# Kernel optimization log

Hardware: AMD Instinct MI355X
Metric: run time of the kernel (lower is better)

Reference implementation:

```python
import jax, jax.numpy as jnp
import numpy as np

B, T, D1, D2, DM, V, K = 2, 512, 256, 128, 1024, 32000, 4
SCALE = 0.05  # keep tanh/sigmoid out of full saturation with randn params


def setup_inputs() -> dict:
    key = jax.random.key(0)
    ks = jax.random.split(key, 7)
    s = lambda k, shape: SCALE * jax.random.normal(k, shape, dtype=jnp.float32)
    return {
        "gc": jax.random.normal(ks[0], (B, T, D1), dtype=jnp.float32),
        "H": s(ks[1], (K, DM, D1)),
        "U": s(ks[2], (K, D2, D1)),
        "v": s(ks[3], (V, D2)),
        "u": s(ks[4], (K, D1)),
        "b": s(ks[5], (V, K)),
        "emb": s(ks[6], (V, DM)),
    }


def reference(gc, H, U, v, u, b, emb):
    # gc: (B,T,D1)
    hc = jnp.tanh(jnp.einsum('kdi,bti->btkd', H, gc))        # (B,T,K,DM)
    tU = jnp.tanh(jnp.einsum('kji,bti->btkj', U, gc))        # (B,T,K,D2)
    # token- and context-dependent gate logits: (B,T,V,K)
    lc = (jnp.einsum('vj,btkj->btvk', v, tU)
          + jnp.einsum('ki,bti->btk', u, gc)[:, :, None, :]
          + b[None, None])
    gamma = jax.nn.sigmoid(lc[..., :K - 1])                  # (B,T,V,3)
    g0, g1, g2 = gamma[..., 0], gamma[..., 1], gamma[..., 2]
    # sigmoid-tree mixture priors: (B,T,V,K)
    pi = jnp.stack([g0 * g1, g0 * (1.0 - g1),
                    (1.0 - g0) * g2, (1.0 - g0) * (1.0 - g2)], axis=-1)
    # contract hc with embeddings per gate FIRST (avoids btikj blow-up),
    # then weight by pi -- same math as the original pi (x) emb outer product.
    dots = jnp.einsum('btkd,vd->btvk', hc, emb)              # (B,T,V,K)
    logits = jnp.sum(pi * dots, axis=-1)                     # (B,T,V)
    return jax.nn.softmax(logits, axis=-1)
```

## Files before the change

### kernel.cpp

```cpp
#include <hip/hip_runtime.h>
#include <math.h>

namespace {

typedef _Float16 f16;
typedef _Float16 f16x8 __attribute__((ext_vector_type(8)));
typedef float    f32x4 __attribute__((ext_vector_type(4)));

constexpr int kBT = 1024, kD1 = 256, kD2 = 128, kDM = 1024, kV = 32000, kK = 4;
constexpr int AR = kBT * kK;
constexpr int ROWS_H = kK * kDM;
constexpr int ROWS_U = kK * kD2;
constexpr int ROWS_ALL = ROWS_H + ROWS_U + kK;
constexpr int HALF_ROWS = ROWS_ALL / 2;

__global__ __launch_bounds__(256) void prep_gemm(
    const float* __restrict__ gc, const float* __restrict__ Hm,
    const float* __restrict__ Um, const float* __restrict__ um,
    f16* __restrict__ hc, f16* __restrict__ tu, float* __restrict__ ug)
{
    __shared__ float sgc[8][kD1];
    const int btBase = blockIdx.x * 8;
    for (int idx = threadIdx.x; idx < 8 * kD1; idx += 256)
        sgc[idx / kD1][idx % kD1] = gc[(size_t)btBase * kD1 + idx];
    __syncthreads();

    const int rStart = blockIdx.y * HALF_ROWS;
    const int rEnd   = rStart + HALF_ROWS;
    for (int r = rStart + (int)threadIdx.x; r < rEnd; r += 256) {
        const float* wrow;
        if (r < ROWS_H)               wrow = Hm + (size_t)r * kD1;
        else if (r < ROWS_H + ROWS_U) wrow = Um + (size_t)(r - ROWS_H) * kD1;
        else                          wrow = um + (size_t)(r - ROWS_H - ROWS_U) * kD1;

        float acc[8] = {0.f,0.f,0.f,0.f,0.f,0.f,0.f,0.f};
        for (int i = 0; i < kD1; i += 4) {
            const float4 w = *reinterpret_cast<const float4*>(wrow + i);
            #pragma unroll
            for (int b = 0; b < 8; ++b) {
                const float4 g = *reinterpret_cast<const float4*>(&sgc[b][i]);
                acc[b] = fmaf(w.x, g.x, acc[b]);
                acc[b] = fmaf(w.y, g.y, acc[b]);
                acc[b] = fmaf(w.z, g.z, acc[b]);
                acc[b] = fmaf(w.w, g.w, acc[b]);
            }
        }
        #pragma unroll
        for (int b = 0; b < 8; ++b) {
            const int bt = btBase + b;
            if (r < ROWS_H) {
                const int k = r >> 10, d = r & 1023;
                hc[((size_t)(bt * kK + k) << 10) + d] = (f16)tanhf(acc[b]);
            } else if (r < ROWS_H + ROWS_U) {
                const int r2 = r - ROWS_H;
                const int k = r2 >> 7, j = r2 & 127;
                tu[(size_t)(bt * kK + k) * kD2 + j] = (f16)tanhf(acc[b]);
            } else {
                ug[bt * kK + (r - ROWS_H - ROWS_U)] = acc[b];
            }
        }
    }
}

__global__ __launch_bounds__(256) void cvt_kernel(
    const float* __restrict__ src, f16* __restrict__ dst, int n8)
{
    const int i = blockIdx.x * 256 + threadIdx.x;
    if (i >= n8) return;
    const float4 x0 = *reinterpret_cast<const float4*>(src + (size_t)i * 8);
    const float4 x1 = *reinterpret_cast<const float4*>(src + (size_t)i * 8 + 4);
    union { f16 h[8]; uint4 v; } u;
    u.h[0] = (f16)x0.x; u.h[1] = (f16)x0.y; u.h[2] = (f16)x0.z; u.h[3] = (f16)x0.w;
    u.h[4] = (f16)x1.x; u.h[5] = (f16)x1.y; u.h[6] = (f16)x1.z; u.h[7] = (f16)x1.w;
    *reinterpret_cast<uint4*>(dst + (size_t)i * 8) = u.v;
}

__global__ __launch_bounds__(256, 2) void fused_mfma(
    const f16* __restrict__ hc,  const f16* __restrict__ tu,
    const f16* __restrict__ v16, const f16* __restrict__ e16,
    const float* __restrict__ ug, const float* __restrict__ bmat,
    float* __restrict__ out)
{
    __shared__ __align__(16) f16 sA[128 * 64];
    __shared__ __align__(16) f16 sB[128 * 64];

    const int tid  = threadIdx.x;
    const int lane = tid & 63;
    const int wave = tid >> 6;
    const int fr = lane & 15, fq = lane >> 4;
    const int wrow = wave >> 1, wcol = wave & 1;
    const int aRowBase = blockIdx.x * 128;
    const int vBase    = blockIdx.y * 128;

    const int srow = lane >> 3;
    const int scol = ((lane & 7) ^ srow) * 8;

    auto stage = [&](const f16* __restrict__ g, f16* ldsbuf, int rowBase,
                     int stride, int dBase) {
        #pragma unroll
        for (int i = 0; i < 4; ++i) {
            const int c = wave * 4 + i;
            const f16* src = g + (size_t)(rowBase + c * 8 + srow) * stride + dBase + scol;
            f16* dst = ldsbuf + c * 512;
            __builtin_amdgcn_global_load_lds(
                (const __attribute__((address_space(1))) void*)src,
                (__attribute__((address_space(3))) void*)dst, 16, 0, 0);
        }
    };

    auto mmStep = [&](f32x4 (&acc)[4][4]) {
        #pragma unroll
        for (int kk = 0; kk < 2; ++kk) {
            f16x8 a[4], b[4];
            #pragma unroll
            for (int m = 0; m < 4; ++m) {
                const int r = wrow * 64 + m * 16 + fr;
                const int ps = (kk * 4 + fq) ^ (r & 7);
                a[m] = *reinterpret_cast<const f16x8*>(sA + r * 64 + ps * 8);
            }
            #pragma unroll
            for (int n = 0; n < 4; ++n) {
                const int r = wcol * 64 + n * 16 + fr;
                const int ps = (kk * 4 + fq) ^ (r & 7);
                b[n] = *reinterpret_cast<const f16x8*>(sB + r * 64 + ps * 8);
            }
            #pragma unroll
            for (int m = 0; m < 4; ++m)
                #pragma unroll
                for (int n = 0; n < 4; ++n)
                    acc[m][n] = __builtin_amdgcn_mfma_f32_16x16x32_f16(
                        a[m], b[n], acc[m][n], 0, 0, 0);
        }
    };

    f32x4 acc[4][4];
    const f32x4 zz = {0.f, 0.f, 0.f, 0.f};

    #pragma unroll
    for (int m = 0; m < 4; ++m)
        #pragma unroll
        for (int n = 0; n < 4; ++n) acc[m][n] = zz;

    for (int t = 0; t < kD2 / 64; ++t) {
        stage(tu,  sA, aRowBase, kD2, t * 64);
        stage(v16, sB, vBase,    kD2, t * 64);
        __syncthreads();
        mmStep(acc);
        __syncthreads();
    }

    float pi[4][4][4];
    #pragma unroll
    for (int m = 0; m < 4; ++m) {
        const int bt = blockIdx.x * 32 + wrow * 16 + m * 4 + fq;
        const float4 ugv = *reinterpret_cast<const float4*>(ug + bt * 4);
        #pragma unroll
        for (int n = 0; n < 4; ++n) {
            const int v = vBase + wcol * 64 + n * 16 + fr;
            const float4 bb = *reinterpret_cast<const float4*>(bmat + (size_t)v * 4);
            const float l0 = acc[m][n][0] + ugv.x + bb.x;
            const float l1 = acc[m][n][1] + ugv.y + bb.y;
            const float l2 = acc[m][n][2] + ugv.z + bb.z;
            const float g0 = 1.f / (1.f + __expf(-l0));
            const float g1 = 1.f / (1.f + __expf(-l1));
            const float g2 = 1.f / (1.f + __expf(-l2));
            pi[m][n][0] = g0 * g1;
            pi[m][n][1] = g0 * (1.f - g1);
            pi[m][n][2] = (1.f - g0) * g2;
            pi[m][n][3] = (1.f - g0) * (1.f - g2);
        }
    }

    #pragma unroll
    for (int m = 0; m < 4; ++m)
        #pragma unroll
        for (int n = 0; n < 4; ++n) acc[m][n] = zz;

    for (int t = 0; t < kDM / 64; ++t) {
        stage(hc,  sA, aRowBase, kDM, t * 64);
        stage(e16, sB, vBase,    kDM, t * 64);
        __syncthreads();
        mmStep(acc);
        __syncthreads();
    }

    #pragma unroll
    for (int m = 0; m < 4; ++m) {
        const int bt = blockIdx.x * 32 + wrow * 16 + m * 4 + fq;
        #pragma unroll
        for (int n = 0; n < 4; ++n) {
            const int v = vBase + wcol * 64 + n * 16 + fr;
            float lg = pi[m][n][0] * acc[m][n][0] + pi[m][n][1] * acc[m][n][1]
                     + pi[m][n][2] * acc[m][n][2] + pi[m][n][3] * acc[m][n][3];
            out[(size_t)bt * kV + v] = lg;
        }
    }
}

__global__ __launch_bounds__(256) void softmax_kernel(float* __restrict__ out)
{
    __shared__ float red[4];
    float* row = out + (size_t)blockIdx.x * kV;
    const int tid = threadIdx.x;

    float mx = -1e30f;
    for (int i = tid * 4; i < kV; i += 1024) {
        const float4 x = *reinterpret_cast<const float4*>(row + i);
        mx = fmaxf(mx, fmaxf(fmaxf(x.x, x.y), fmaxf(x.z, x.w)));
    }
    #pragma unroll
    for (int o = 1; o < 64; o <<= 1) mx = fmaxf(mx, __shfl_xor(mx, o));
    if ((tid & 63) == 0) red[tid >> 6] = mx;
    __syncthreads();
    mx = fmaxf(fmaxf(red[0], red[1]), fmaxf(red[2], red[3]));
    __syncthreads();

    float s = 0.f;
    for (int i = tid * 4; i < kV; i += 1024) {
        const float4 x = *reinterpret_cast<const float4*>(row + i);
        s += __expf(x.x - mx) + __expf(x.y - mx) + __expf(x.z - mx) + __expf(x.w - mx);
    }
    #pragma unroll
    for (int o = 1; o < 64; o <<= 1) s += __shfl_xor(s, o);
    if ((tid & 63) == 0) red[tid >> 6] = s;
    __syncthreads();
    s = red[0] + red[1] + red[2] + red[3];
    const float inv = 1.f / s;

    for (int i = tid * 4; i < kV; i += 1024) {
        const float4 x = *reinterpret_cast<const float4*>(row + i);
        float4 y;
        y.x = __expf(x.x - mx) * inv;
        y.y = __expf(x.y - mx) * inv;
        y.z = __expf(x.z - mx) * inv;
        y.w = __expf(x.w - mx) * inv;
        *reinterpret_cast<float4*>(row + i) = y;
    }
}

}

extern "C" void kernel_launch(void* const* d_in, const int* in_sizes, int n_in,
                              void* d_out, int out_size, void* d_ws, size_t ws_size,
                              hipStream_t stream)
{
    (void)in_sizes; (void)n_in; (void)out_size; (void)ws_size;
    const float* gc   = (const float*)d_in[0];
    const float* Hm   = (const float*)d_in[1];
    const float* Um   = (const float*)d_in[2];
    const float* vmat = (const float*)d_in[3];
    const float* um   = (const float*)d_in[4];
    const float* bmat = (const float*)d_in[5];
    const float* emb  = (const float*)d_in[6];
    float* out = (float*)d_out;

    size_t off = 0;
    auto take = [&](size_t bytes) -> char* {
        char* p = (char*)d_ws + off;
        off += (bytes + 255) & ~(size_t)255;
        return p;
    };
    f16*   hc  = (f16*)  take((size_t)AR * kDM * 2);
    f16*   tu  = (f16*)  take((size_t)AR * kD2 * 2);
    f16*   v16 = (f16*)  take((size_t)kV * kD2 * 2);
    f16*   e16 = (f16*)  take((size_t)kV * kDM * 2);
    float* ug  = (float*)take((size_t)AR * 4);

    prep_gemm<<<dim3(kBT / 8, 2), 256, 0, stream>>>(gc, Hm, Um, um, hc, tu, ug);
    cvt_kernel<<<(kV * kD2 / 8 + 255) / 256, 256, 0, stream>>>(vmat, v16, kV * kD2 / 8);
    cvt_kernel<<<(kV * kDM / 8 + 255) / 256, 256, 0, stream>>>(emb, e16, kV * kDM / 8);
    fused_mfma<<<dim3(AR / 128, kV / 128), 256, 0, stream>>>(
        hc, tu, v16, e16, ug, bmat, out);
    softmax_kernel<<<dim3(kBT), 256, 0, stream>>>(out);
}
```

Before: 576.4 us.

## Enlarge MFMA tiles to 256x256 with 4-stage async LDS pipeline and XCD remap

The fused GEMM kernel moves from 128x128 tiles with 256 threads to 256x256 tiles with 512 threads. The K-tile shrinks to 32 and a 4-buffer ring of global_load_lds transfers is prefetched two tiles ahead, with explicit vmcnt waits and a single barrier per phase. The gate and embedding GEMMs now share one continuous pipeline. A 1D grid is remapped so each XCD handles contiguous row blocks for L2 reuse, and the pi weights are packed to fp16 to cut register pressure. The larger accumulator footprint risks register spills or lower occupancy, and the fp16 pi adds a small precision loss.

```diff
diff --git a/kernel.cpp b/kernel.cpp
--- a/kernel.cpp
+++ b/kernel.cpp
@@ -75,123 +75,149 @@
     *reinterpret_cast<uint4*>(dst + (size_t)i * 8) = u.v;
 }
 
-__global__ __launch_bounds__(256, 2) void fused_mfma(
+__device__ __forceinline__ uint packf16x2(float a, float b) {
+    union { f16 h[2]; uint u; } z;
+    z.h[0] = (f16)a; z.h[1] = (f16)b;
+    return z.u;
+}
+
+__global__ __launch_bounds__(512, 2) void fused_mfma(
     const f16* __restrict__ hc,  const f16* __restrict__ tu,
     const f16* __restrict__ v16, const f16* __restrict__ e16,
     const float* __restrict__ ug, const float* __restrict__ bmat,
     float* __restrict__ out)
 {
-    __shared__ __align__(16) f16 sA[128 * 64];
-    __shared__ __align__(16) f16 sB[128 * 64];
+    __shared__ __align__(16) f16 sA[4][256 * 32];
+    __shared__ __align__(16) f16 sB[4][256 * 32];
+
+    constexpr int NT_G = kD2 / 32;
+    constexpr int NT_TOT = NT_G + kDM / 32;
 
     const int tid  = threadIdx.x;
     const int lane = tid & 63;
     const int wave = tid >> 6;
     const int fr = lane & 15, fq = lane >> 4;
-    const int wrow = wave >> 1, wcol = wave & 1;
-    const int aRowBase = blockIdx.x * 128;
-    const int vBase    = blockIdx.y * 128;
-
-    const int srow = lane >> 3;
-    const int scol = ((lane & 7) ^ srow) * 8;
-
-    auto stage = [&](const f16* __restrict__ g, f16* ldsbuf, int rowBase,
-                     int stride, int dBase) {
-        #pragma unroll
-        for (int i = 0; i < 4; ++i) {
-            const int c = wave * 4 + i;
-            const f16* src = g + (size_t)(rowBase + c * 8 + srow) * stride + dBase + scol;
-            f16* dst = ldsbuf + c * 512;
+    const int wrow = wave >> 2, wcol = wave & 3;
+
+    const int wg  = blockIdx.x;
+    const int xcd = wg & 7;
+    const int idx = wg >> 3;
+    const int bx  = xcd * 2 + idx / 125;
+    const int by  = idx % 125;
+    const int aRowBase = bx * 256;
+    const int vBase    = by * 256;
+
+    const int srow16 = lane >> 2;
+    const int sslot  = lane & 3;
+    const int swzc   = ((sslot ^ (srow16 & 3) ^ ((srow16 >> 2) & 3))) * 8;
+
+    const int pslot = fq ^ (fr & 3) ^ ((fr >> 2) & 3);
+
+    auto stage_tile = [&](int t) {
+        if (t >= NT_TOT) return;
+        const bool g = (t < NT_G);
+        const f16* A = g ? tu  : hc;
+        const f16* B = g ? v16 : e16;
+        const int stride = g ? kD2 : kDM;
+        const int dB = g ? t * 32 : (t - NT_G) * 32;
+        const int q = t & 3;
+        #pragma unroll
+        for (int i = 0; i < 2; ++i) {
+            const int c = wave * 2 + i;
+            const f16* srcA = A + (size_t)(aRowBase + c * 16 + srow16) * stride + dB + swzc;
             __builtin_amdgcn_global_load_lds(
-                (const __attribute__((address_space(1))) void*)src,
-                (__attribute__((address_space(3))) void*)dst, 16, 0, 0);
+                (const __attribute__((address_space(1))) void*)srcA,
+                (__attribute__((address_space(3))) void*)(&sA[q][c * 512]), 16, 0, 0);
+            const f16* srcB = B + (size_t)(vBase + c * 16 + srow16) * stride + dB + swzc;
+            __builtin_amdgcn_global_load_lds(
+                (const __attribute__((address_space(1))) void*)srcB,
+                (__attribute__((address_space(3))) void*)(&sB[q][c * 512]), 16, 0, 0);
         }
     };
 
-    auto mmStep = [&](f32x4 (&acc)[4][4]) {
-        #pragma unroll
-        for (int kk = 0; kk < 2; ++kk) {
-            f16x8 a[4], b[4];
-            #pragma unroll
-            for (int m = 0; m < 4; ++m) {
-                const int r = wrow * 64 + m * 16 + fr;
-                const int ps = (kk * 4 + fq) ^ (r & 7);
-                a[m] = *reinterpret_cast<const f16x8*>(sA + r * 64 + ps * 8);
-            }
+#define PHASE(T, ACC, VM)                                                     \
+    {                                                                         \
+        stage_tile((T) + 2);                                                  \
+        asm volatile("s_waitcnt vmcnt(" VM ")" ::: "memory");                 \
+        __builtin_amdgcn_s_barrier();                                         \
+        asm volatile("" ::: "memory");                                        \
+        const f16* __restrict__ pa = &sA[(T) & 3][0];                         \
+        const f16* __restrict__ pb = &sB[(T) & 3][0];                         \
+        f16x8 bfr[4];                                                         \
+        _Pragma("unroll")                                                     \
+        for (int n = 0; n < 4; ++n) {                                         \
+            const int r = wcol * 64 + n * 16 + fr;                            \
+            bfr[n] = *reinterpret_cast<const f16x8*>(pb + r * 32 + pslot * 8);\
+        }                                                                     \
+        _Pragma("unroll")                                                     \
+        for (int m = 0; m < 8; ++m) {                                         \
+            const int r = wrow * 128 + m * 16 + fr;                           \
+            const f16x8 afr =                                                 \
+                *reinterpret_cast<const f16x8*>(pa + r * 32 + pslot * 8);     \
+            _Pragma("unroll")                                                 \
+            for (int n = 0; n < 4; ++n)                                       \
+                ACC[m][n] = __builtin_amdgcn_mfma_f32_16x16x32_f16(           \
+                    afr, bfr[n], ACC[m][n], 0, 0, 0);                         \
+        }                                                                     \
+    }
+
+    f32x4 gacc[8][4];
+    const f32x4 zz = {0.f, 0.f, 0.f, 0.f};
+    #pragma unroll
+    for (int m = 0; m < 8; ++m)
+        #pragma unroll
+        for (int n = 0; n < 4; ++n) gacc[m][n] = zz;
+
+    stage_tile(0);
+    stage_tile(1);
+    for (int t = 0; t < NT_G; ++t) PHASE(t, gacc, "8");
+
+    uint pi01[8][4], pi23[8][4];
+    {
+        const int btB = bx * 64 + wrow * 32;
+        #pragma unroll
+        for (int m = 0; m < 8; ++m) {
+            const float4 ugv = *reinterpret_cast<const float4*>(ug + (btB + m * 4 + fq) * 4);
             #pragma unroll
             for (int n = 0; n < 4; ++n) {
-                const int r = wcol * 64 + n * 16 + fr;
-                const int ps = (kk * 4 + fq) ^ (r & 7);
-                b[n] = *reinterpret_cast<const f16x8*>(sB + r * 64 + ps * 8);
+                const int v = vBase + wcol * 64 + n * 16 + fr;
+                const float4 bb = *reinterpret_cast<const float4*>(bmat + (size_t)v * 4);
+                const float l0 = gacc[m][n][0] + ugv.x + bb.x;
+                const float l1 = gacc[m][n][1] + ugv.y + bb.y;
+                const float l2 = gacc[m][n][2] + ugv.z + bb.z;
+                const float g0 = 1.f / (1.f + __expf(-l0));
+                const float g1 = 1.f / (1.f + __expf(-l1));
+                const float g2 = 1.f / (1.f + __expf(-l2));
+                pi01[m][n] = packf16x2(g0 * g1, g0 * (1.f - g1));
+                pi23[m][n] = packf16x2((1.f - g0) * g2, (1.f - g0) * (1.f - g2));
             }
-            #pragma unroll
-            for (int m = 0; m < 4; ++m)
-                #pragma unroll
-                for (int n = 0; n < 4; ++n)
-                    acc[m][n] = __builtin_amdgcn_mfma_f32_16x16x32_f16(
-                        a[m], b[n], acc[m][n], 0, 0, 0);
-        }
-    };
-
-    f32x4 acc[4][4];
-    const f32x4 zz = {0.f, 0.f, 0.f, 0.f};
-
-    #pragma unroll
-    for (int m = 0; m < 4; ++m)
-        #pragma unroll
-        for (int n = 0; n < 4; ++n) acc[m][n] = zz;
-
-    for (int t = 0; t < kD2 / 64; ++t) {
-        stage(tu,  sA, aRowBase, kD2, t * 64);
-        stage(v16, sB, vBase,    kD2, t * 64);
-        __syncthreads();
-        mmStep(acc);
-        __syncthreads();
-    }
-
-    float pi[4][4][4];
-    #pragma unroll
-    for (int m = 0; m < 4; ++m) {
-        const int bt = blockIdx.x * 32 + wrow * 16 + m * 4 + fq;
-        const float4 ugv = *reinterpret_cast<const float4*>(ug + bt * 4);
+        }
+    }
+
+    f32x4 dacc[8][4];
+    #pragma unroll
+    for (int m = 0; m < 8; ++m)
+        #pragma unroll
+        for (int n = 0; n < 4; ++n) dacc[m][n] = zz;
+
+    for (int t = NT_G; t <= NT_TOT - 3; ++t) PHASE(t, dacc, "8");
+    PHASE(NT_TOT - 2, dacc, "4");
+    PHASE(NT_TOT - 1, dacc, "0");
+#undef PHASE
+
+    const int btB = bx * 64 + wrow * 32;
+    #pragma unroll
+    for (int m = 0; m < 8; ++m) {
+        const int bt = btB + m * 4 + fq;
         #pragma unroll
         for (int n = 0; n < 4; ++n) {
             const int v = vBase + wcol * 64 + n * 16 + fr;
-            const float4 bb = *reinterpret_cast<const float4*>(bmat + (size_t)v * 4);
-            const float l0 = acc[m][n][0] + ugv.x + bb.x;
-            const float l1 = acc[m][n][1] + ugv.y + bb.y;
-            const float l2 = acc[m][n][2] + ugv.z + bb.z;
-            const float g0 = 1.f / (1.f + __expf(-l0));
-            const float g1 = 1.f / (1.f + __expf(-l1));
-            const float g2 = 1.f / (1.f + __expf(-l2));
-            pi[m][n][0] = g0 * g1;
-            pi[m][n][1] = g0 * (1.f - g1);
-            pi[m][n][2] = (1.f - g0) * g2;
-            pi[m][n][3] = (1.f - g0) * (1.f - g2);
-        }
-    }
-
-    #pragma unroll
-    for (int m = 0; m < 4; ++m)
-        #pragma unroll
-        for (int n = 0; n < 4; ++n) acc[m][n] = zz;
-
-    for (int t = 0; t < kDM / 64; ++t) {
-        stage(hc,  sA, aRowBase, kDM, t * 64);
-        stage(e16, sB, vBase,    kDM, t * 64);
-        __syncthreads();
-        mmStep(acc);
-        __syncthreads();
-    }
-
-    #pragma unroll
-    for (int m = 0; m < 4; ++m) {
-        const int bt = blockIdx.x * 32 + wrow * 16 + m * 4 + fq;
-        #pragma unroll
-        for (int n = 0; n < 4; ++n) {
-            const int v = vBase + wcol * 64 + n * 16 + fr;
-            float lg = pi[m][n][0] * acc[m][n][0] + pi[m][n][1] * acc[m][n][1]
-                     + pi[m][n][2] * acc[m][n][2] + pi[m][n][3] * acc[m][n][3];
+            union { uint u; f16 h[2]; } p01, p23;
+            p01.u = pi01[m][n]; p23.u = pi23[m][n];
+            const float lg = (float)p01.h[0] * dacc[m][n][0]
+                           + (float)p01.h[1] * dacc[m][n][1]
+                           + (float)p23.h[0] * dacc[m][n][2]
+                           + (float)p23.h[1] * dacc[m][n][3];
             out[(size_t)bt * kV + v] = lg;
         }
     }
@@ -269,7 +295,7 @@
     prep_gemm<<<dim3(kBT / 8, 2), 256, 0, stream>>>(gc, Hm, Um, um, hc, tu, ug);
     cvt_kernel<<<(kV * kD2 / 8 + 255) / 256, 256, 0, stream>>>(vmat, v16, kV * kD2 / 8);
     cvt_kernel<<<(kV * kDM / 8 + 255) / 256, 256, 0, stream>>>(emb, e16, kV * kDM / 8);
-    fused_mfma<<<dim3(AR / 128, kV / 128), 256, 0, stream>>>(
+    fused_mfma<<<dim3((AR / 256) * (kV / 256)), 512, 0, stream>>>(
         hc, tu, v16, e16, ug, bmat, out);
     softmax_kernel<<<dim3(kBT), 256, 0, stream>>>(out);
 }
```

After: 727.0 us. +26.1%, slower.
